# Kernel tuning notes

Measured on AMD Instinct MI355X. Metric: run time of the kernel, lower is better.

Reference implementation:

```python
import jax, jax.numpy as jnp
import numpy as np

V, E, H, L, B, T = 50000, 512, 512, 32, 64, 512


def _lstm_dir(xg, w_hh, reverse):
    # xg: [B,T,4H] precomputed input-to-gate projections (+ biases)
    b, t, g4 = xg.shape
    h_dim = g4 // 4
    def step(carry, xt):
        h, c = carry
        g = xt + h @ w_hh.T  # [B,4H], PyTorch gate order i,f,g,o
        i, f, gg, o = jnp.split(g, 4, axis=-1)
        c = jax.nn.sigmoid(f) * c + jax.nn.sigmoid(i) * jnp.tanh(gg)
        h = jax.nn.sigmoid(o) * jnp.tanh(c)
        return (h, c), h
    init = (jnp.zeros((b, h_dim), xg.dtype), jnp.zeros((b, h_dim), xg.dtype))
    _, hs = jax.lax.scan(step, init, jnp.swapaxes(xg, 0, 1), reverse=reverse)
    return jnp.swapaxes(hs, 0, 1)  # [B,T,H]


def _bilstm(x, w_ih0, w_ih1, w_hh, b_ih, b_hh):
    w_ihs = (w_ih0, w_ih1)
    for l in range(2):
        outs = []
        for d in range(2):  # 0=forward, 1=backward
            xg = jnp.einsum('bti,gi->btg', x, w_ihs[l][d]) + b_ih[l, d] + b_hh[l, d]
            outs.append(_lstm_dir(xg, w_hh[l, d], reverse=(d == 1)))
        x = jnp.concatenate(outs, axis=-1)  # [B,T,2H]
    return x


def _crf_nll(emissions, tags, start, end, trans):
    # pytorch-crf: returns sum log-likelihood; module returns its negation.
    emit = jnp.take_along_axis(emissions, tags[..., None], axis=-1)[..., 0]  # [B,T]
    num = (start[tags[:, 0]] + emit.sum(1)
           + trans[tags[:, :-1], tags[:, 1:]].sum(1) + end[tags[:, -1]])
    alpha0 = start + emissions[:, 0]  # [B,L]
    def step(alpha, e_t):
        s = alpha[:, :, None] + trans[None] + e_t[:, None, :]  # [B,L,L]
        return jax.nn.logsumexp(s, axis=1), None
    alpha, _ = jax.lax.scan(step, alpha0, jnp.swapaxes(emissions[:, 1:], 0, 1))
    denom = jax.nn.logsumexp(alpha + end, axis=-1)  # [B]
    return -(num - denom).sum()


def setup_inputs() -> dict:
    key = jax.random.key(0)
    ks = jax.random.split(key, 13)
    s = 0.05
    emb = jax.random.normal(ks[0], (V, E), jnp.float32) * s
    emb = emb.at[0].set(0.0)  # padding_idx=0
    return {
        'datas': jax.random.randint(ks[1], (B, T), 0, V, jnp.int32),
        'labels': jax.random.randint(ks[2], (B, T), 0, L, jnp.int32),
        'emb': emb,
        'w_ih0': jax.random.normal(ks[3], (2, 4 * H, E), jnp.float32) * s,
        'w_ih1': jax.random.normal(ks[4], (2, 4 * H, 2 * H), jnp.float32) * s,
        'w_hh': jax.random.normal(ks[5], (2, 2, 4 * H, H), jnp.float32) * s,
        'b_ih': jax.random.normal(ks[6], (2, 2, 4 * H), jnp.float32) * s,
        'b_hh': jax.random.normal(ks[7], (2, 2, 4 * H), jnp.float32) * s,
        'w_out': jax.random.normal(ks[8], (2 * H, L), jnp.float32) * s,
        'b_out': jax.random.normal(ks[9], (L,), jnp.float32) * s,
        'crf_start': jax.random.normal(ks[10], (L,), jnp.float32) * s,
        'crf_end': jax.random.normal(ks[11], (L,), jnp.float32) * s,
        'crf_trans': jax.random.normal(ks[12], (L, L), jnp.float32) * s,
    }


def reference(datas, labels, emb, w_ih0, w_ih1, w_hh, b_ih, b_hh, w_out, b_out,
              crf_start, crf_end, crf_trans):
    x = emb[datas]  # [B,T,E]
    h = _bilstm(x, w_ih0, w_ih1, w_hh, b_ih, b_hh)  # [B,T,2H]; dropout=0 (eval)
    emissions = h @ w_out + b_out  # [B,T,L]
    return _crf_nll(emissions, labels, crf_start, crf_end, crf_trans)
```

## Files before the change

### kernel.cpp

```cpp
#include <hip/hip_runtime.h>

typedef unsigned short ushort_t;
typedef unsigned long long u64_t;
typedef __attribute__((ext_vector_type(8))) short short8;
typedef __attribute__((ext_vector_type(4))) short short4v;
typedef __attribute__((ext_vector_type(4))) float floatx4;


__device__ __forceinline__ float bf2f(ushort_t u) {
  unsigned x = ((unsigned)u) << 16;
  return __builtin_bit_cast(float, x);
}
__device__ __forceinline__ ushort_t f2bf(float f) {
  unsigned x = __builtin_bit_cast(unsigned, f);
  x += 0x7FFFu + ((x >> 16) & 1u);
  return (ushort_t)(x >> 16);
}
__device__ __forceinline__ float sigf(float x) { return 1.0f / (1.0f + __expf(-x)); }
__device__ __forceinline__ float tanhf_(float x) { return 1.0f - 2.0f / (__expf(2.0f * x) + 1.0f); }

static const size_t OFF_A    = 0;
static const size_t OFF_OUT0 = 67108864;
static const size_t OFF_XG   = 134217728;
static const size_t OFF_WIH0 = 167772160;
static const size_t OFF_WIH1 = 171966464;
static const size_t OFF_BIAS = 180355072;
static const size_t OFF_WOUT = 180387840;
static const size_t OFF_HC   = 180453376;
static const size_t OFF_CST  = 181501952;
static const size_t OFF_BAR  = 182026240;
static const size_t OFF_NUM  = 182059008;
static const size_t OFF_PERB = 182059264;
static const size_t OFF_END  = 182059520;

__global__ void prep_embed(const int* __restrict__ datas, const float* __restrict__ emb,
                           ushort_t* __restrict__ x_bf,
                           const float* __restrict__ w_ih0, const float* __restrict__ w_ih1,
                           const float* __restrict__ b_ih, const float* __restrict__ b_hh,
                           const float* __restrict__ w_out,
                           ushort_t* __restrict__ wih0_bf, ushort_t* __restrict__ wih1_bf,
                           float* __restrict__ bias, ushort_t* __restrict__ wout_bf) {
  int idx = blockIdx.x * 256 + threadIdx.x;
  int stride = gridDim.x * 256;
  for (int i = idx; i < 2097152; i += stride) {
    int row = i >> 6, sub = i & 63;
    int tok = datas[row];
    const float4* ep = (const float4*)(emb + (size_t)tok * 512 + sub * 8);
    float4 f0 = ep[0], f1 = ep[1];
    short8 v;
    v[0] = (short)f2bf(f0.x); v[1] = (short)f2bf(f0.y);
    v[2] = (short)f2bf(f0.z); v[3] = (short)f2bf(f0.w);
    v[4] = (short)f2bf(f1.x); v[5] = (short)f2bf(f1.y);
    v[6] = (short)f2bf(f1.z); v[7] = (short)f2bf(f1.w);
    *(short8*)(x_bf + (size_t)row * 512 + sub * 8) = v;
  }
  for (int i = idx; i < 2097152; i += stride) wih0_bf[i] = f2bf(w_ih0[i]);
  for (int i = idx; i < 4194304; i += stride) wih1_bf[i] = f2bf(w_ih1[i]);
  for (int i = idx; i < 8192; i += stride) bias[i] = b_ih[i] + b_hh[i];
  for (int i = idx; i < 32768; i += stride) {
    int j = i & 7, Ls = (i >> 3) & 63, kb = (i >> 9) & 31, nt = i >> 14;
    int n = nt * 16 + (Ls & 15);
    int k = kb * 32 + ((Ls >> 4) & 3) * 8 + j;
    wout_bf[i] = f2bf(w_out[k * 32 + n]);
  }
}

__device__ __forceinline__ void gemm_body(ushort_t* alds, ushort_t* blds, int gid, int tid,
                                          const ushort_t* __restrict__ A, int K,
                                          const ushort_t* __restrict__ W,
                                          const float* __restrict__ biasL,
                                          ushort_t* __restrict__ xg0,
                                          ushort_t* __restrict__ xg1,
                                          int t00, int t01) {
  int dir = gid >> 9, r = gid & 511;
  int mt = r & 31, ntt = r >> 5;
  int t0 = dir ? t01 : t00;
  const ushort_t* Bm = W + (size_t)dir * 2048 * K;
  const float* bptr = biasL + dir * 2048;
  ushort_t* xg = dir ? xg1 : xg0;
  int bm0 = mt * 128, bn0 = ntt * 128;
  int L = tid & 63, w = tid >> 6;
  int wm = w & 1, wn = w >> 1;
  floatx4 acc[4][4] = {};
  for (int k0 = 0; k0 < K; k0 += 32) {
    __syncthreads();
    #pragma unroll
    for (int rep = 0; rep < 2; rep++) {
      int slot = rep * 256 + tid;
      int t8 = slot >> 6, Ls = slot & 63;
      int col = k0 + (Ls >> 4) * 8;
      int mp = bm0 + t8 * 16 + (Ls & 15);
      int Arow = (mp >> 6) * 512 + t0 + (mp & 63);
      *(short8*)&alds[slot * 8] = *(const short8*)&A[(size_t)Arow * K + col];
      int rowb = bn0 + t8 * 16 + (Ls & 15);
      *(short8*)&blds[slot * 8] = *(const short8*)&Bm[(size_t)rowb * K + col];
    }
    __syncthreads();
    short8 af[4];
    #pragma unroll
    for (int a = 0; a < 4; a++) af[a] = *(const short8*)&alds[((wm * 4 + a) * 64 + L) * 8];
    #pragma unroll
    for (int bq = 0; bq < 4; bq++) {
      short8 bfr = *(const short8*)&blds[((wn * 4 + bq) * 64 + L) * 8];
      #pragma unroll
      for (int a = 0; a < 4; a++)
        acc[a][bq] = __builtin_amdgcn_mfma_f32_16x16x32_bf16(af[a], bfr, acc[a][bq], 0, 0, 0);
    }
  }
  int lm = L >> 4, ln = L & 15;
  #pragma unroll
  for (int bq = 0; bq < 4; bq++) {
    int n = bn0 + (wn * 4 + bq) * 16 + ln;
    float bv = bptr[n];
    int nidx = ((n & 511) << 2) + (n >> 9);
    #pragma unroll
    for (int a = 0; a < 4; a++) {
      #pragma unroll
      for (int rr = 0; rr < 4; rr++) {
        int m = bm0 + (wm * 4 + a) * 16 + lm * 4 + rr;
        int b = m >> 6, ts = m & 63;
        xg[((size_t)(ts * 64 + b)) * 2048 + nidx] = f2bf(acc[a][bq][rr] + bv);
      }
    }
  }
}

__global__ __launch_bounds__(256) void gemm_chunk(const ushort_t* __restrict__ A, int K,
                                                  const ushort_t* __restrict__ W,
                                                  const float* __restrict__ biasL,
                                                  ushort_t* __restrict__ xg0c,
                                                  ushort_t* __restrict__ xg1c,
                                                  int t00, int t01) {
  __shared__ alignas(16) ushort_t alds[512 * 8];
  __shared__ alignas(16) ushort_t blds[512 * 8];
  gemm_body(alds, blds, blockIdx.x, threadIdx.x, A, K, W, biasL, xg0c, xg1c, t00, t01);
}

__device__ __forceinline__ void lstm_body(ushort_t* wlds, int bid, int tid,
                                          const ushort_t* __restrict__ xg0c,
                                          const ushort_t* __restrict__ xg1c,
                                          const float* __restrict__ whh_f,
                                          ushort_t* __restrict__ hcL,
                                          float* __restrict__ cstL,
                                          ushort_t* __restrict__ outL,
                                          int* __restrict__ barF, int c) {
  int d = bid >> 5, g = bid & 31, j0 = g * 16;
  int L = tid & 63, w = tid >> 6;
  const float* wptr = whh_f + (size_t)d * 2048 * 512;
  #pragma unroll
  for (int it = 0; it < 16; it++) {
    int slot = it * 256 + tid;
    int q = slot >> 10, kb = (slot >> 6) & 15, Ls = slot & 63;
    int gcol = q * 512 + j0 + (Ls & 15);
    int k = kb * 32 + (Ls >> 4) * 8;
    const float* src = wptr + (size_t)gcol * 512 + k;
    float4 f0 = *(const float4*)src;
    float4 f1 = *(const float4*)(src + 4);
    short8 v;
    v[0] = (short)f2bf(f0.x); v[1] = (short)f2bf(f0.y);
    v[2] = (short)f2bf(f0.z); v[3] = (short)f2bf(f0.w);
    v[4] = (short)f2bf(f1.x); v[5] = (short)f2bf(f1.y);
    v[6] = (short)f2bf(f1.z); v[7] = (short)f2bf(f1.w);
    *(short8*)&wlds[slot * 8] = v;
  }
  __syncthreads();
  const ushort_t* xgd = d ? xg1c : xg0c;
  ushort_t* hcd = hcL + (size_t)d * 2 * 32768;
  int* flg = barF + d * 2048;
  int* myflag = flg + (g * 4 + w) * 16;
  const int* pollp = flg + ((L & 31) * 4 + w) * 16;
  bool pact = (L < 32);
  int q8 = L >> 4, jj = L & 15;
  int mbase = w * 16 + q8 * 4;
  int wslot = ((w * 16 + (g >> 1)) * 64 + q8 * 4 + 16 * ((g & 1) * 2 + (jj >> 3))) * 8 + (jj & 7);
  int rbase = (w * 16 * 64 + L) * 8;
  float cv[4];
  #pragma unroll
  for (int rr = 0; rr < 4; rr++) cv[rr] = cstL[(size_t)d * 32768 + (mbase + rr) * 512 + j0 + jj];

  auto ldxg = [&](int sl2, ushort_t dst[4][4]) {
    int ts2 = d ? (63 - sl2) : sl2;
    #pragma unroll
    for (int rr = 0; rr < 4; rr++) {
      const short4v* xrow = (const short4v*)(xgd + ((size_t)(ts2 * 64 + mbase + rr)) * 2048
                                             + ((j0 + jj) << 2));
      short4v v = *xrow;
      #pragma unroll
      for (int q = 0; q < 4; q++) dst[q][rr] = (ushort_t)v[q];
    }
  };

  ushort_t xgu[4][4];
  ldxg(0, xgu);

  for (int sl = 0; sl < 64; sl++) {
    int s = c * 64 + sl;
    int t = d ? (511 - s) : s;
    const u64_t* h64 = (const u64_t*)(hcd + (size_t)(s & 1) * 32768);
    unsigned* h32w = (unsigned*)(hcd + (size_t)((s + 1) & 1) * 32768);
    int b64 = rbase >> 2;
    u64_t hv[32];
    #pragma unroll
    for (int kb = 0; kb < 16; kb++) {
      hv[2 * kb]     = __hip_atomic_load(h64 + b64 + kb * 128,     __ATOMIC_RELAXED, __HIP_MEMORY_SCOPE_AGENT);
      hv[2 * kb + 1] = __hip_atomic_load(h64 + b64 + kb * 128 + 1, __ATOMIC_RELAXED, __HIP_MEMORY_SCOPE_AGENT);
    }
    floatx4 acc[4] = {};
    #pragma unroll
    for (int kb = 0; kb < 16; kb++) {
      union { u64_t u[2]; short8 v; } pk;
      pk.u[0] = hv[2 * kb];
      pk.u[1] = hv[2 * kb + 1];
      short8 a = pk.v;
      #pragma unroll
      for (int q = 0; q < 4; q++) {
        short8 bfr = *(const short8*)&wlds[((q * 16 + kb) * 64 + L) * 8];
        acc[q] = __builtin_amdgcn_mfma_f32_16x16x32_bf16(a, bfr, acc[q], 0, 0, 0);
      }
    }
    ushort_t hbv[4];
    #pragma unroll
    for (int rr = 0; rr < 4; rr++) {
      float ii = acc[0][rr] + bf2f(xgu[0][rr]);
      float ff = acc[1][rr] + bf2f(xgu[1][rr]);
      float gg = acc[2][rr] + bf2f(xgu[2][rr]);
      float oo = acc[3][rr] + bf2f(xgu[3][rr]);
      float cc = sigf(ff) * cv[rr] + sigf(ii) * tanhf_(gg);
      cv[rr] = cc;
      hbv[rr] = f2bf(sigf(oo) * tanhf_(cc));
    }
    bool evn = (jj & 1) == 0;
    unsigned pk4[4];
    #pragma unroll
    for (int rr = 0; rr < 4; rr++) {
      unsigned mine = (unsigned)hbv[rr];
      unsigned nb = (unsigned)__shfl_xor((int)mine, 1, 64);
      pk4[rr] = mine | (nb << 16);
      if (evn)
        __hip_atomic_store(h32w + ((wslot + rr * 8) >> 1), pk4[rr],
                           __ATOMIC_RELAXED, __HIP_MEMORY_SCOPE_AGENT);
    }
    if (sl != 63) {
      asm volatile("s_waitcnt vmcnt(0)" ::: "memory");
      if (L == 0)
        __hip_atomic_store(myflag, s + 1, __ATOMIC_RELAXED, __HIP_MEMORY_SCOPE_AGENT);
      if (evn) {
        #pragma unroll
        for (int rr = 0; rr < 4; rr++) {
          int m = mbase + rr;
          *(unsigned*)&outL[((size_t)m * 512 + t) * 1024 + (d << 9) + j0 + jj] = pk4[rr];
        }
      }
      ldxg(sl + 1, xgu);
      int target = s + 1, guard = 0;
      int f0 = pact ? __hip_atomic_load(pollp, __ATOMIC_RELAXED, __HIP_MEMORY_SCOPE_AGENT)
                    : target;
      while (guard < (1 << 17)) {
        int f1 = pact ? __hip_atomic_load(pollp, __ATOMIC_RELAXED, __HIP_MEMORY_SCOPE_AGENT)
                      : target;
        if (__ballot(f0 >= target) == ~0ULL) break;
        f0 = f1;
        guard++;
      }
    } else {
      if (evn) {
        #pragma unroll
        for (int rr = 0; rr < 4; rr++) {
          int m = mbase + rr;
          *(unsigned*)&outL[((size_t)m * 512 + t) * 1024 + (d << 9) + j0 + jj] = pk4[rr];
        }
      }
    }
  }
  #pragma unroll
  for (int rr = 0; rr < 4; rr++) cstL[(size_t)d * 32768 + (mbase + rr) * 512 + j0 + jj] = cv[rr];
}

__global__ __launch_bounds__(256) void lstm_chunk(const ushort_t* __restrict__ xg0c,
                                                  const ushort_t* __restrict__ xg1c,
                                                  const float* __restrict__ whh_f,
                                                  ushort_t* __restrict__ hcL,
                                                  float* __restrict__ cstL,
                                                  ushort_t* __restrict__ outL,
                                                  int* __restrict__ barF, int c) {
  __shared__ alignas(16) ushort_t wlds[32768];
  lstm_body(wlds, blockIdx.x, threadIdx.x, xg0c, xg1c, whh_f, hcL, cstL, outL, barF, c);
}

__global__ __launch_bounds__(256) void fused_chunk(
    const ushort_t* __restrict__ l_xg0, const ushort_t* __restrict__ l_xg1,
    const float* __restrict__ whh_f, ushort_t* __restrict__ hcL,
    float* __restrict__ cstL, ushort_t* __restrict__ outL,
    int* __restrict__ barF, int c,
    const ushort_t* __restrict__ g_A, int g_K,
    const ushort_t* __restrict__ g_W, const float* __restrict__ g_bias,
    ushort_t* __restrict__ g_xg0, ushort_t* __restrict__ g_xg1,
    int g_t00, int g_t01) {
  __shared__ alignas(16) ushort_t lds[32768];
  if (blockIdx.x < 64) {
    lstm_body(lds, blockIdx.x, threadIdx.x, l_xg0, l_xg1, whh_f, hcL, cstL, outL, barF, c);
  } else {
    gemm_body(lds, lds + 4096, blockIdx.x - 64, threadIdx.x,
              g_A, g_K, g_W, g_bias, g_xg0, g_xg1, g_t00, g_t01);
  }
}

__global__ __launch_bounds__(256) void emis_kernel(const ushort_t* __restrict__ out1,
                                                   const ushort_t* __restrict__ wout_bf,
                                                   const float* __restrict__ b_out,
                                                   float* __restrict__ emis) {
  int tid = threadIdx.x, L = tid & 63, w = tid >> 6;
  int bm0 = blockIdx.x * 128;
  int q8 = L >> 4, ln = L & 15;
  floatx4 acc[2][2] = {};
  #pragma unroll 4
  for (int kb = 0; kb < 32; kb++) {
    short8 a0 = *(const short8*)&out1[(size_t)(bm0 + (w * 2 + 0) * 16 + ln) * 1024 + kb * 32 + q8 * 8];
    short8 a1 = *(const short8*)&out1[(size_t)(bm0 + (w * 2 + 1) * 16 + ln) * 1024 + kb * 32 + q8 * 8];
    #pragma unroll
    for (int nt = 0; nt < 2; nt++) {
      short8 bfr = *(const short8*)&wout_bf[((size_t)(nt * 32 + kb) * 64 + L) * 8];
      acc[0][nt] = __builtin_amdgcn_mfma_f32_16x16x32_bf16(a0, bfr, acc[0][nt], 0, 0, 0);
      acc[1][nt] = __builtin_amdgcn_mfma_f32_16x16x32_bf16(a1, bfr, acc[1][nt], 0, 0, 0);
    }
  }
  #pragma unroll
  for (int mt = 0; mt < 2; mt++) {
    #pragma unroll
    for (int nt = 0; nt < 2; nt++) {
      int n = nt * 16 + ln;
      float bv = b_out[n];
      #pragma unroll
      for (int rr = 0; rr < 4; rr++) {
        int m = bm0 + (w * 2 + mt) * 16 + q8 * 4 + rr;
        emis[(size_t)m * 32 + n] = acc[mt][nt][rr] + bv;
      }
    }
  }
}

__global__ __launch_bounds__(64) void fwd_kernel(const int* __restrict__ labels,
                                                 const float* __restrict__ emis,
                                                 const float* __restrict__ trans,
                                                 const float* __restrict__ cstart,
                                                 const float* __restrict__ cend,
                                                 float* __restrict__ perb) {
  int b = blockIdx.x, tid = threadIdx.x, j = tid & 31;
  float sn = 0.f;
  for (int t = tid; t < 512; t += 64) {
    int tag = labels[b * 512 + t];
    sn += emis[(size_t)(b * 512 + t) * 32 + tag];
    if (t < 511) sn += trans[tag * 32 + labels[b * 512 + t + 1]];
  }
  #pragma unroll
  for (int off = 32; off > 0; off >>= 1) sn += __shfl_xor(sn, off, 64);
  sn += cstart[labels[b * 512]] + cend[labels[b * 512 + 511]];
  float etr[32];
  #pragma unroll
  for (int i = 0; i < 32; i++) etr[i] = __expf(trans[i * 32 + j]);
  float alpha = cstart[j] + emis[(size_t)(b * 512) * 32 + j];
  float e_cur = emis[(size_t)(b * 512 + 1) * 32 + j];
  for (int t = 1; t < 512; t++) {
    float e_nx = (t < 511) ? emis[(size_t)(b * 512 + t + 1) * 32 + j] : 0.f;
    float mA = alpha;
    mA = fmaxf(mA, __shfl_xor(mA, 1, 32));
    mA = fmaxf(mA, __shfl_xor(mA, 2, 32));
    mA = fmaxf(mA, __shfl_xor(mA, 4, 32));
    mA = fmaxf(mA, __shfl_xor(mA, 8, 32));
    mA = fmaxf(mA, __shfl_xor(mA, 16, 32));
    float p = __expf(alpha - mA);
    float s0 = 0.f, s1 = 0.f, s2 = 0.f, s3 = 0.f;
    #pragma unroll
    for (int i = 0; i < 32; i += 4) {
      s0 = fmaf(__shfl(p, i, 32),     etr[i],     s0);
      s1 = fmaf(__shfl(p, i + 1, 32), etr[i + 1], s1);
      s2 = fmaf(__shfl(p, i + 2, 32), etr[i + 2], s2);
      s3 = fmaf(__shfl(p, i + 3, 32), etr[i + 3], s3);
    }
    alpha = __logf((s0 + s1) + (s2 + s3)) + mA + e_cur;
    e_cur = e_nx;
  }
  float z = alpha + cend[j];
  float m2 = z;
  #pragma unroll
  for (int off = 16; off > 0; off >>= 1) m2 = fmaxf(m2, __shfl_xor(m2, off, 32));
  float s2r = __expf(z - m2);
  #pragma unroll
  for (int off = 16; off > 0; off >>= 1) s2r += __shfl_xor(s2r, off, 32);
  if (tid == 0) perb[b] = sn - (__logf(s2r) + m2);
}

__global__ void final_kernel(const float* __restrict__ perb, float* __restrict__ out) {
  int tid = threadIdx.x;
  float s = perb[tid];
  #pragma unroll
  for (int off = 32; off > 0; off >>= 1) s += __shfl_xor(s, off, 64);
  if (tid == 0) out[0] = -s;
}

extern "C" void kernel_launch(void* const* d_in, const int* in_sizes, int n_in,
                              void* d_out, int out_size, void* d_ws, size_t ws_size,
                              hipStream_t stream) {
  (void)in_sizes; (void)n_in; (void)out_size;
  const int* datas = (const int*)d_in[0];
  const int* labels = (const int*)d_in[1];
  const float* emb = (const float*)d_in[2];
  const float* w_ih0 = (const float*)d_in[3];
  const float* w_ih1 = (const float*)d_in[4];
  const float* w_hh = (const float*)d_in[5];
  const float* b_ih = (const float*)d_in[6];
  const float* b_hh = (const float*)d_in[7];
  const float* w_out = (const float*)d_in[8];
  const float* b_out = (const float*)d_in[9];
  const float* cstart = (const float*)d_in[10];
  const float* cend = (const float*)d_in[11];
  const float* ctrans = (const float*)d_in[12];

  char* ws = (char*)d_ws;
  ushort_t* x_bf = (ushort_t*)(ws + OFF_A);
  ushort_t* out1 = (ushort_t*)(ws + OFF_A);
  ushort_t* out0 = (ushort_t*)(ws + OFF_OUT0);
  ushort_t* xA0 = (ushort_t*)(ws + OFF_XG);
  ushort_t* xA1 = (ushort_t*)(ws + OFF_XG + 16777216);
  ushort_t* xB0a = (ushort_t*)(ws + OFF_A + 33554432);
  ushort_t* xB0b = (ushort_t*)(ws + OFF_A + 50331648);
  ushort_t* xB1a = (ushort_t*)(ws + OFF_END);
  ushort_t* xB1b = (ushort_t*)(ws + OFF_END + 16777216);
  bool big = ws_size >= OFF_END + 33554432ull;
  float* emis = (float*)(ws + OFF_XG);
  ushort_t* wih0_bf = (ushort_t*)(ws + OFF_WIH0);
  ushort_t* wih1_bf = (ushort_t*)(ws + OFF_WIH1);
  float* bias = (float*)(ws + OFF_BIAS);
  ushort_t* wout_bf = (ushort_t*)(ws + OFF_WOUT);
  ushort_t* hc0 = (ushort_t*)(ws + OFF_HC);
  ushort_t* hc1 = hc0 + 131072;
  float* cst0 = (float*)(ws + OFF_CST);
  float* cst1 = cst0 + 65536;
  int* bar = (int*)(ws + OFF_BAR);
  float* perb = (float*)(ws + OFF_PERB);

  hipMemsetAsync(ws + OFF_HC, 0, OFF_END - OFF_HC, stream);

  prep_embed<<<8192, 256, 0, stream>>>(datas, emb, x_bf, w_ih0, w_ih1, b_ih, b_hh, w_out,
                                       wih0_bf, wih1_bf, bias, wout_bf);

  gemm_chunk<<<1024, 256, 0, stream>>>(x_bf, 512, wih0_bf, bias, xA0, xA1, 0, 448);
  for (int c = 0; c < 8; c++) {
    ushort_t* r0 = (c & 1) ? xB0a : xA0;
    ushort_t* r1 = (c & 1) ? xB0b : xA1;
    if (c < 7) {
      ushort_t* w0 = ((c + 1) & 1) ? xB0a : xA0;
      ushort_t* w1 = ((c + 1) & 1) ? xB0b : xA1;
      fused_chunk<<<1088, 256, 0, stream>>>(r0, r1, w_hh, hc0, cst0, out0, bar, c,
                                            x_bf, 512, wih0_bf, bias, w0, w1,
                                            (c + 1) * 64, (6 - c) * 64);
    } else {
      lstm_chunk<<<64, 256, 0, stream>>>(r0, r1, w_hh, hc0, cst0, out0, bar, c);
    }
  }

  gemm_chunk<<<1024, 256, 0, stream>>>(out0, 1024, wih1_bf, bias + 4096, xA0, xA1, 0, 448);
  for (int c = 0; c < 8; c++) {
    if (big) {
      ushort_t* r0 = (c & 1) ? xB1a : xA0;
      ushort_t* r1 = (c & 1) ? xB1b : xA1;
      if (c < 7) {
        ushort_t* w0 = ((c + 1) & 1) ? xB1a : xA0;
        ushort_t* w1 = ((c + 1) & 1) ? xB1b : xA1;
        fused_chunk<<<1088, 256, 0, stream>>>(r0, r1, w_hh + 2097152, hc1, cst1, out1,
                                              bar + 4096, c,
                                              out0, 1024, wih1_bf, bias + 4096, w0, w1,
                                              (c + 1) * 64, (6 - c) * 64);
      } else {
        lstm_chunk<<<64, 256, 0, stream>>>(r0, r1, w_hh + 2097152, hc1, cst1, out1,
                                           bar + 4096, c);
      }
    } else {
      lstm_chunk<<<64, 256, 0, stream>>>(xA0, xA1, w_hh + 2097152, hc1, cst1, out1,
                                         bar + 4096, c);
      if (c < 7)
        gemm_chunk<<<1024, 256, 0, stream>>>(out0, 1024, wih1_bf, bias + 4096, xA0, xA1,
                                             (c + 1) * 64, (6 - c) * 64);
    }
  }

  emis_kernel<<<256, 256, 0, stream>>>(out1, wout_bf, b_out, emis);
  fwd_kernel<<<64, 64, 0, stream>>>(labels, emis, ctrans, cstart, cend, perb);
  final_kernel<<<1, 64, 0, stream>>>(perb, (float*)d_out);
}
```

Measured before the change: 5.582 ms.

## Pre-pack recurrent weights to bf16 once and simplify xg layout and polling

Adds a pre-pass in prep_embed that converts w_hh to bf16 in the exact LDS slot order, so each LSTM chunk block copies its slice with plain 16-byte loads instead of converting fp32 every launch (16 launches). The gate-projection output drops the interleaved column layout for plain row-major order, so the LSTM loads four strided scalars per row instead of one 4-short vector. The spin-wait loop is reduced to a single atomic load per iteration. The cost is extra workspace and a larger prep pass, plus less coalesced xg reads in the recurrent step.

```diff
diff --git a/kernel.cpp b/kernel.cpp
--- a/kernel.cpp
+++ b/kernel.cpp
@@ -3,7 +3,6 @@
 typedef unsigned short ushort_t;
 typedef unsigned long long u64_t;
 typedef __attribute__((ext_vector_type(8))) short short8;
-typedef __attribute__((ext_vector_type(4))) short short4v;
 typedef __attribute__((ext_vector_type(4))) float floatx4;
 
 
@@ -31,15 +30,17 @@
 static const size_t OFF_BAR  = 182026240;
 static const size_t OFF_NUM  = 182059008;
 static const size_t OFF_PERB = 182059264;
-static const size_t OFF_END  = 182059520;
+static const size_t OFF_WHH  = 182059520;
+static const size_t OFF_XB1  = 190448128;
 
 __global__ void prep_embed(const int* __restrict__ datas, const float* __restrict__ emb,
                            ushort_t* __restrict__ x_bf,
                            const float* __restrict__ w_ih0, const float* __restrict__ w_ih1,
                            const float* __restrict__ b_ih, const float* __restrict__ b_hh,
-                           const float* __restrict__ w_out,
+                           const float* __restrict__ w_out, const float* __restrict__ w_hh,
                            ushort_t* __restrict__ wih0_bf, ushort_t* __restrict__ wih1_bf,
-                           float* __restrict__ bias, ushort_t* __restrict__ wout_bf) {
+                           float* __restrict__ bias, ushort_t* __restrict__ wout_bf,
+                           ushort_t* __restrict__ whh_pp, int do_pp) {
   int idx = blockIdx.x * 256 + threadIdx.x;
   int stride = gridDim.x * 256;
   for (int i = idx; i < 2097152; i += stride) {
@@ -62,6 +63,15 @@
     int n = nt * 16 + (Ls & 15);
     int k = kb * 32 + ((Ls >> 4) & 3) * 8 + j;
     wout_bf[i] = f2bf(w_out[k * 32 + n]);
+  }
+  if (do_pp) {
+    for (int i = idx; i < 4194304; i += stride) {
+      int j = i & 7, slot = (i >> 3) & 4095, g = (i >> 15) & 31, d = (i >> 20) & 1, l = i >> 21;
+      int q = slot >> 10, kb = (slot >> 6) & 15, Ls = slot & 63;
+      int gcol = q * 512 + g * 16 + (Ls & 15);
+      int k = kb * 32 + ((Ls >> 4) & 3) * 8 + j;
+      whh_pp[i] = f2bf(w_hh[(((size_t)(l * 2 + d) * 2048) + gcol) * 512 + k]);
+    }
   }
 }
 
@@ -112,14 +122,13 @@
   for (int bq = 0; bq < 4; bq++) {
     int n = bn0 + (wn * 4 + bq) * 16 + ln;
     float bv = bptr[n];
-    int nidx = ((n & 511) << 2) + (n >> 9);
     #pragma unroll
     for (int a = 0; a < 4; a++) {
       #pragma unroll
       for (int rr = 0; rr < 4; rr++) {
         int m = bm0 + (wm * 4 + a) * 16 + lm * 4 + rr;
         int b = m >> 6, ts = m & 63;
-        xg[((size_t)(ts * 64 + b)) * 2048 + nidx] = f2bf(acc[a][bq][rr] + bv);
+        xg[((size_t)(ts * 64 + b)) * 2048 + n] = f2bf(acc[a][bq][rr] + bv);
       }
     }
   }
@@ -140,28 +149,38 @@
                                           const ushort_t* __restrict__ xg0c,
                                           const ushort_t* __restrict__ xg1c,
                                           const float* __restrict__ whh_f,
+                                          const ushort_t* __restrict__ whh_pp,
                                           ushort_t* __restrict__ hcL,
                                           float* __restrict__ cstL,
                                           ushort_t* __restrict__ outL,
                                           int* __restrict__ barF, int c) {
   int d = bid >> 5, g = bid & 31, j0 = g * 16;
   int L = tid & 63, w = tid >> 6;
-  const float* wptr = whh_f + (size_t)d * 2048 * 512;
-  #pragma unroll
-  for (int it = 0; it < 16; it++) {
-    int slot = it * 256 + tid;
-    int q = slot >> 10, kb = (slot >> 6) & 15, Ls = slot & 63;
-    int gcol = q * 512 + j0 + (Ls & 15);
-    int k = kb * 32 + (Ls >> 4) * 8;
-    const float* src = wptr + (size_t)gcol * 512 + k;
-    float4 f0 = *(const float4*)src;
-    float4 f1 = *(const float4*)(src + 4);
-    short8 v;
-    v[0] = (short)f2bf(f0.x); v[1] = (short)f2bf(f0.y);
-    v[2] = (short)f2bf(f0.z); v[3] = (short)f2bf(f0.w);
-    v[4] = (short)f2bf(f1.x); v[5] = (short)f2bf(f1.y);
-    v[6] = (short)f2bf(f1.z); v[7] = (short)f2bf(f1.w);
-    *(short8*)&wlds[slot * 8] = v;
+  if (whh_pp) {
+    const ushort_t* src = whh_pp + (size_t)(d * 32 + g) * 32768;
+    #pragma unroll
+    for (int it = 0; it < 16; it++) {
+      int slot = it * 256 + tid;
+      *(short8*)&wlds[slot * 8] = *(const short8*)&src[slot * 8];
+    }
+  } else {
+    const float* wptr = whh_f + (size_t)d * 2048 * 512;
+    #pragma unroll
+    for (int it = 0; it < 16; it++) {
+      int slot = it * 256 + tid;
+      int q = slot >> 10, kb = (slot >> 6) & 15, Ls = slot & 63;
+      int gcol = q * 512 + j0 + (Ls & 15);
+      int k = kb * 32 + (Ls >> 4) * 8;
+      const float* src = wptr + (size_t)gcol * 512 + k;
+      float4 f0 = *(const float4*)src;
+      float4 f1 = *(const float4*)(src + 4);
+      short8 v;
+      v[0] = (short)f2bf(f0.x); v[1] = (short)f2bf(f0.y);
+      v[2] = (short)f2bf(f0.z); v[3] = (short)f2bf(f0.w);
+      v[4] = (short)f2bf(f1.x); v[5] = (short)f2bf(f1.y);
+      v[6] = (short)f2bf(f1.z); v[7] = (short)f2bf(f1.w);
+      *(short8*)&wlds[slot * 8] = v;
+    }
   }
   __syncthreads();
   const ushort_t* xgd = d ? xg1c : xg0c;
@@ -182,11 +201,9 @@
     int ts2 = d ? (63 - sl2) : sl2;
     #pragma unroll
     for (int rr = 0; rr < 4; rr++) {
-      const short4v* xrow = (const short4v*)(xgd + ((size_t)(ts2 * 64 + mbase + rr)) * 2048
-                                             + ((j0 + jj) << 2));
-      short4v v = *xrow;
+      const ushort_t* xrow = xgd + ((size_t)(ts2 * 64 + mbase + rr)) * 2048 + j0 + jj;
       #pragma unroll
-      for (int q = 0; q < 4; q++) dst[q][rr] = (ushort_t)v[q];
+      for (int q = 0; q < 4; q++) dst[q][rr] = xrow[q * 512];
     }
   };
 
@@ -253,13 +270,10 @@
       }
       ldxg(sl + 1, xgu);
       int target = s + 1, guard = 0;
-      int f0 = pact ? __hip_atomic_load(pollp, __ATOMIC_RELAXED, __HIP_MEMORY_SCOPE_AGENT)
-                    : target;
       while (guard < (1 << 17)) {
-        int f1 = pact ? __hip_atomic_load(pollp, __ATOMIC_RELAXED, __HIP_MEMORY_SCOPE_AGENT)
-                      : target;
-        if (__ballot(f0 >= target) == ~0ULL) break;
-        f0 = f1;
+        int f = pact ? __hip_atomic_load(pollp, __ATOMIC_RELAXED, __HIP_MEMORY_SCOPE_AGENT)
+                     : target;
+        if (__ballot(f >= target) == ~0ULL) break;
         guard++;
       }
     } else {
@@ -279,17 +293,19 @@
 __global__ __launch_bounds__(256) void lstm_chunk(const ushort_t* __restrict__ xg0c,
                                                   const ushort_t* __restrict__ xg1c,
                                                   const float* __restrict__ whh_f,
+                                                  const ushort_t* __restrict__ whh_pp,
                                                   ushort_t* __restrict__ hcL,
                                                   float* __restrict__ cstL,
                                                   ushort_t* __restrict__ outL,
                                                   int* __restrict__ barF, int c) {
   __shared__ alignas(16) ushort_t wlds[32768];
-  lstm_body(wlds, blockIdx.x, threadIdx.x, xg0c, xg1c, whh_f, hcL, cstL, outL, barF, c);
+  lstm_body(wlds, blockIdx.x, threadIdx.x, xg0c, xg1c, whh_f, whh_pp, hcL, cstL, outL, barF, c);
 }
 
 __global__ __launch_bounds__(256) void fused_chunk(
     const ushort_t* __restrict__ l_xg0, const ushort_t* __restrict__ l_xg1,
-    const float* __restrict__ whh_f, ushort_t* __restrict__ hcL,
+    const float* __restrict__ whh_f, const ushort_t* __restrict__ whh_pp,
+    ushort_t* __restrict__ hcL,
     float* __restrict__ cstL, ushort_t* __restrict__ outL,
     int* __restrict__ barF, int c,
     const ushort_t* __restrict__ g_A, int g_K,
@@ -298,7 +314,7 @@
     int g_t00, int g_t01) {
   __shared__ alignas(16) ushort_t lds[32768];
   if (blockIdx.x < 64) {
-    lstm_body(lds, blockIdx.x, threadIdx.x, l_xg0, l_xg1, whh_f, hcL, cstL, outL, barF, c);
+    lstm_body(lds, blockIdx.x, threadIdx.x, l_xg0, l_xg1, whh_f, whh_pp, hcL, cstL, outL, barF, c);
   } else {
     gemm_body(lds, lds + 4096, blockIdx.x - 64, threadIdx.x,
               g_A, g_K, g_W, g_bias, g_xg0, g_xg1, g_t00, g_t01);
@@ -424,9 +440,10 @@
   ushort_t* xA1 = (ushort_t*)(ws + OFF_XG + 16777216);
   ushort_t* xB0a = (ushort_t*)(ws + OFF_A + 33554432);
   ushort_t* xB0b = (ushort_t*)(ws + OFF_A + 50331648);
-  ushort_t* xB1a = (ushort_t*)(ws + OFF_END);
-  ushort_t* xB1b = (ushort_t*)(ws + OFF_END + 16777216);
-  bool big = ws_size >= OFF_END + 33554432ull;
+  ushort_t* xB1a = (ushort_t*)(ws + OFF_XB1);
+  ushort_t* xB1b = (ushort_t*)(ws + OFF_XB1 + 16777216);
+  bool pp_ok = ws_size >= OFF_WHH + 8388608ull;
+  bool big = ws_size >= OFF_XB1 + 33554432ull;
   float* emis = (float*)(ws + OFF_XG);
   ushort_t* wih0_bf = (ushort_t*)(ws + OFF_WIH0);
   ushort_t* wih1_bf = (ushort_t*)(ws + OFF_WIH1);
@@ -438,11 +455,15 @@
   float* cst1 = cst0 + 65536;
   int* bar = (int*)(ws + OFF_BAR);
   float* perb = (float*)(ws + OFF_PERB);
-
-  hipMemsetAsync(ws + OFF_HC, 0, OFF_END - OFF_HC, stream);
+  ushort_t* whh_pp = pp_ok ? (ushort_t*)(ws + OFF_WHH) : (ushort_t*)nullptr;
+  ushort_t* pp0 = pp_ok ? whh_pp : (ushort_t*)nullptr;
+  ushort_t* pp1 = pp_ok ? (whh_pp + 2097152) : (ushort_t*)nullptr;
+
+  hipMemsetAsync(ws + OFF_HC, 0, OFF_WHH - OFF_HC, stream);
 
   prep_embed<<<8192, 256, 0, stream>>>(datas, emb, x_bf, w_ih0, w_ih1, b_ih, b_hh, w_out,
-                                       wih0_bf, wih1_bf, bias, wout_bf);
+                                       w_hh, wih0_bf, wih1_bf, bias, wout_bf,
+                                       whh_pp, pp_ok ? 1 : 0);
 
   gemm_chunk<<<1024, 256, 0, stream>>>(x_bf, 512, wih0_bf, bias, xA0, xA1, 0, 448);
   for (int c = 0; c < 8; c++) {
@@ -451,11 +472,11 @@
     if (c < 7) {
       ushort_t* w0 = ((c + 1) & 1) ? xB0a : xA0;
       ushort_t* w1 = ((c + 1) & 1) ? xB0b : xA1;
-      fused_chunk<<<1088, 256, 0, stream>>>(r0, r1, w_hh, hc0, cst0, out0, bar, c,
+      fused_chunk<<<1088, 256, 0, stream>>>(r0, r1, w_hh, pp0, hc0, cst0, out0, bar, c,
                                             x_bf, 512, wih0_bf, bias, w0, w1,
                                             (c + 1) * 64, (6 - c) * 64);
     } else {
-      lstm_chunk<<<64, 256, 0, stream>>>(r0, r1, w_hh, hc0, cst0, out0, bar, c);
+      lstm_chunk<<<64, 256, 0, stream>>>(r0, r1, w_hh, pp0, hc0, cst0, out0, bar, c);
     }
   }
 
@@ -467,16 +488,16 @@
       if (c < 7) {
         ushort_t* w0 = ((c + 1) & 1) ? xB1a : xA0;
         ushort_t* w1 = ((c + 1) & 1) ? xB1b : xA1;
-        fused_chunk<<<1088, 256, 0, stream>>>(r0, r1, w_hh + 2097152, hc1, cst1, out1,
+        fused_chunk<<<1088, 256, 0, stream>>>(r0, r1, w_hh + 2097152, pp1, hc1, cst1, out1,
                                               bar + 4096, c,
                                               out0, 1024, wih1_bf, bias + 4096, w0, w1,
                                               (c + 1) * 64, (6 - c) * 64);
       } else {
-        lstm_chunk<<<64, 256, 0, stream>>>(r0, r1, w_hh + 2097152, hc1, cst1, out1,
+        lstm_chunk<<<64, 256, 0, stream>>>(r0, r1, w_hh + 2097152, pp1, hc1, cst1, out1,
                                            bar + 4096, c);
       }
     } else {
-      lstm_chunk<<<64, 256, 0, stream>>>(xA0, xA1, w_hh + 2097152, hc1, cst1, out1,
+      lstm_chunk<<<64, 256, 0, stream>>>(xA0, xA1, w_hh + 2097152, pp1, hc1, cst1, out1,
                                          bar + 4096, c);
       if (c < 7)
         gemm_chunk<<<1024, 256, 0, stream>>>(out0, 1024, wih1_bf, bias + 4096, xA0, xA1,
```

After: 4.845 ms. 13.2% less time.
